# Kernel tuning notes

Hardware: AMD Instinct MI355X
Metric: run time of the kernel (lower is better)

The kernel has to match this reference:

```python
import math
import jax, jax.numpy as jnp
import numpy as np


def setup_inputs() -> dict:
    key = jax.random.key(0)
    k1, k2, k3, k4 = jax.random.split(key, 4)
    B, K, D = 131072, 64, 8
    NC = D * (D + 1) // 2  # 36
    pi = jax.random.uniform(k1, (B, K), dtype=jnp.float32)
    mu = jax.random.normal(k2, (K, D), dtype=jnp.float32)
    # 'ALREADY CONSTRAINED' Cholesky entries: keep them positive (uniform),
    # +0.1 offset keeps diagonal safely away from 0 for the log.
    L_constrained = jax.random.uniform(k3, (K, NC), dtype=jnp.float32) + 0.1
    target = jax.random.normal(k4, (B, D), dtype=jnp.float32)
    return {"pi": pi, "mu": mu, "L_constrained": L_constrained, "target": target}


def reference(pi, mu, L_constrained, target):
    B, K = pi.shape
    D = mu.shape[1]
    norm_const = -0.5 * D * math.log(2.0 * math.pi)
    ti, tj = np.tril_indices(D)
    # scatter packed cholesky into dense lower-triangular (K, D, D)
    L = jnp.zeros((K, D, D), dtype=target.dtype).at[:, ti, tj].set(L_constrained)
    diff = target[:, None, :] - mu[None, :, :]          # (B, K, D)
    # batch over components, treat B as multiple RHS: L (K,D,D) @ z = b (K,D,B)
    b = jnp.transpose(diff, (1, 2, 0))                   # (K, D, B)
    z = jax.scipy.linalg.solve_triangular(L, b, lower=True)  # (K, D, B)
    M = jnp.sum(z * z, axis=1)                           # (K, B) Mahalanobis^2
    log_dets = jnp.sum(jnp.log(jnp.diagonal(L, axis1=-2, axis2=-1)), axis=-1)  # (K,)
    log_probs = norm_const - log_dets[:, None] - 0.5 * M  # (K, B)
    weighted = log_probs.T + jnp.log(pi + 1e-10)          # (B, K)
    nll = -jnp.mean(jax.scipy.special.logsumexp(weighted, axis=1))
    return nll
```

## Files before the change

### kernel.cpp

```cpp
#include <hip/hip_runtime.h>
#include <math.h>

#define B_TOTAL 131072
#define K_COMP  64
#define D_DIM   8
#define NC      36
#define NFEAT   96
#define LPSI    104
#define ROWS_PB 128
#define TPW     2

#define NORM_CONST (-7.3515082656373815f)

typedef __attribute__((ext_vector_type(8))) short bf16x8;
typedef __attribute__((ext_vector_type(4))) float f32x4;

static __device__ __forceinline__ unsigned short bf16_rne(float x) {
    unsigned u = __float_as_uint(x);
    u += 0x7FFF + ((u >> 16) & 1);
    return (unsigned short)(u >> 16);
}
static __device__ __forceinline__ float bf16_f32(unsigned short h) {
    return __uint_as_float(((unsigned)h) << 16);
}

__global__ __launch_bounds__(256, 4) void mdn_fused(
        const float* __restrict__ pi,
        const float* __restrict__ mu,
        const float* __restrict__ Lc,
        const float* __restrict__ target,
        float* __restrict__ out) {
    const int tid = threadIdx.x;
    const int lane = tid & 63;
    const int w = tid >> 6;
    const int q = lane >> 4;
    const int n = lane & 15;
    const int rowbase = blockIdx.x * ROWS_PB;

    __shared__ __attribute__((aligned(16))) float Tl[ROWS_PB * D_DIM];
    __shared__ __attribute__((aligned(16))) unsigned short PsiH[K_COMP * LPSI];
    __shared__ __attribute__((aligned(16))) unsigned short PsiL[K_COMP * LPSI];

    ((float4*)Tl)[tid] = ((const float4*)(target + (size_t)rowbase * D_DIM))[tid];

    if (tid < K_COMP) {
        const int k = tid;
        const float* Lk = Lc + k * NC;

        float L[NC];
        float W[NC];
#pragma unroll
        for (int i = 0; i < NC; i++) L[i] = Lk[i];

        float logdet = 0.0f;
#pragma unroll
        for (int i = 0; i < D_DIM; i++) logdet += __logf(L[i * (i + 1) / 2 + i]);

#pragma unroll
        for (int j = 0; j < D_DIM; j++) {
            W[j * (j + 1) / 2 + j] = 1.0f / L[j * (j + 1) / 2 + j];
#pragma unroll
            for (int i = 0; i < D_DIM; i++) {
                if (i > j) {
                    float acc = 0.0f;
#pragma unroll
                    for (int m = 0; m < D_DIM; m++)
                        if (m >= j && m < i)
                            acc += L[i * (i + 1) / 2 + m] * W[m * (m + 1) / 2 + j];
                    W[i * (i + 1) / 2 + j] = -acc / L[i * (i + 1) / 2 + i];
                }
            }
        }

        float P[D_DIM][D_DIM];
#pragma unroll
        for (int a = 0; a < D_DIM; a++)
#pragma unroll
            for (int b = 0; b < D_DIM; b++) {
                float acc = 0.0f;
#pragma unroll
                for (int m = 0; m < D_DIM; m++)
                    if (m >= a && m >= b)
                        acc += W[m * (m + 1) / 2 + a] * W[m * (m + 1) / 2 + b];
                P[a][b] = acc;
            }

        float mv[D_DIM];
#pragma unroll
        for (int i = 0; i < D_DIM; i++) mv[i] = mu[k * D_DIM + i];

        float h[D_DIM];
        float qf = 0.0f;
#pragma unroll
        for (int i = 0; i < D_DIM; i++) {
            float acc = 0.0f;
#pragma unroll
            for (int j = 0; j < D_DIM; j++) acc += P[i][j] * mv[j];
            h[i] = acc;
            qf += mv[i] * acc;
        }
        float g = NORM_CONST - logdet - 0.5f * qf;

        float psi[NFEAT];
#pragma unroll
        for (int e = 0; e < NFEAT; e++) psi[e] = 0.0f;
#pragma unroll
        for (int a = 0; a < D_DIM; a++)
#pragma unroll
            for (int b = 0; b < D_DIM; b++) psi[8 * a + b] = -0.5f * P[a][b];
#pragma unroll
        for (int b = 0; b < D_DIM; b++) psi[64 + b] = h[b];
        psi[72] = g;

#pragma unroll
        for (int e8 = 0; e8 < NFEAT / 8; e8++) {
            bf16x8 vh, vl;
#pragma unroll
            for (int j = 0; j < 8; j++) {
                float v = psi[8 * e8 + j];
                unsigned short hi = bf16_rne(v);
                vh[j] = (short)hi;
                vl[j] = (short)bf16_rne(v - bf16_f32(hi));
            }
            *(bf16x8*)(PsiH + k * LPSI + 8 * e8) = vh;
            *(bf16x8*)(PsiL + k * LPSI + 8 * e8) = vl;
        }
    }
    __syncthreads();

    float lacc = 0.0f;

#pragma unroll 1
    for (int r = 0; r < TPW; r++) {
        const int row0 = (w * TPW + r) * 16;

        float pv[4][4];
#pragma unroll
        for (int reg = 0; reg < 4; reg++) {
            const float* pr = pi + (size_t)(rowbase + row0 + 4 * q + reg) * K_COMP + n;
#pragma unroll
            for (int nt = 0; nt < 4; nt++) pv[reg][nt] = pr[16 * nt];
        }

        const float4* trow = (const float4*)(Tl + (row0 + n) * D_DIM);
        float4 tlo = trow[0], thi = trow[1];
        float tv[D_DIM] = {tlo.x, tlo.y, tlo.z, tlo.w, thi.x, thi.y, thi.z, thi.w};

        float ta0 = (q & 2) ? ((q & 1) ? tlo.w : tlo.z) : ((q & 1) ? tlo.y : tlo.x);
        float ta1 = (q & 2) ? ((q & 1) ? thi.w : thi.z) : ((q & 1) ? thi.y : thi.x);

        bf16x8 Ahi[3], Alo[3];
#pragma unroll
        for (int j = 0; j < D_DIM; j++) {
            float f0 = ta0 * tv[j];
            unsigned short h0 = bf16_rne(f0);
            Ahi[0][j] = (short)h0;
            Alo[0][j] = (short)bf16_rne(f0 - bf16_f32(h0));

            float f1 = ta1 * tv[j];
            unsigned short h1 = bf16_rne(f1);
            Ahi[1][j] = (short)h1;
            Alo[1][j] = (short)bf16_rne(f1 - bf16_f32(h1));

            float f2 = (q == 0) ? tv[j] : ((q == 1 && j == 0) ? 1.0f : 0.0f);
            unsigned short h2 = bf16_rne(f2);
            Ahi[2][j] = (short)h2;
            Alo[2][j] = (short)bf16_rne(f2 - bf16_f32(h2));
        }

        f32x4 acc[4];
#pragma unroll
        for (int nt = 0; nt < 4; nt++) {
            const unsigned short* bh = PsiH + ((16 * nt + n) * LPSI + 8 * q);
            const unsigned short* bl = PsiL + ((16 * nt + n) * LPSI + 8 * q);
            f32x4 a = {0.0f, 0.0f, 0.0f, 0.0f};
#pragma unroll
            for (int ks = 0; ks < 3; ks++) {
                bf16x8 Bh = *(const bf16x8*)(bh + 32 * ks);
                bf16x8 Bl = *(const bf16x8*)(bl + 32 * ks);
                a = __builtin_amdgcn_mfma_f32_16x16x32_bf16(Ahi[ks], Bh, a, 0, 0, 0);
                a = __builtin_amdgcn_mfma_f32_16x16x32_bf16(Alo[ks], Bh, a, 0, 0, 0);
                a = __builtin_amdgcn_mfma_f32_16x16x32_bf16(Ahi[ks], Bl, a, 0, 0, 0);
            }
            acc[nt] = a;
        }

#pragma unroll
        for (int reg = 0; reg < 4; reg++) {
            float c0 = acc[0][reg], c1 = acc[1][reg], c2 = acc[2][reg], c3 = acc[3][reg];
            float mrow = fmaxf(fmaxf(c0, c1), fmaxf(c2, c3));
#pragma unroll
            for (int off = 1; off < 16; off <<= 1)
                mrow = fmaxf(mrow, __shfl_xor(mrow, off));
            float s = (pv[reg][0] + 1e-10f) * __expf(c0 - mrow)
                    + (pv[reg][1] + 1e-10f) * __expf(c1 - mrow)
                    + (pv[reg][2] + 1e-10f) * __expf(c2 - mrow)
                    + (pv[reg][3] + 1e-10f) * __expf(c3 - mrow);
#pragma unroll
            for (int off = 1; off < 16; off <<= 1)
                s += __shfl_xor(s, off);
            float lse = mrow + __logf(s);
            lacc += (n == 0) ? lse : 0.0f;
        }
    }

#pragma unroll
    for (int off = 32; off > 0; off >>= 1) lacc += __shfl_down(lacc, off);
    __shared__ float wsum[4];
    if (lane == 0) wsum[w] = lacc;
    __syncthreads();
    if (tid == 0) {
        atomicAdd(out, (wsum[0] + wsum[1] + wsum[2] + wsum[3]) * (-1.0f / (float)B_TOTAL));
    }
}

extern "C" void kernel_launch(void* const* d_in, const int* in_sizes, int n_in,
                              void* d_out, int out_size, void* d_ws, size_t ws_size,
                              hipStream_t stream) {
    const float* pi  = (const float*)d_in[0];
    const float* mu  = (const float*)d_in[1];
    const float* Lc  = (const float*)d_in[2];
    const float* tgt = (const float*)d_in[3];
    float* out = (float*)d_out;

    mdn_fused<<<B_TOTAL / ROWS_PB, 256, 0, stream>>>(pi, mu, Lc, tgt, out);
}
```

Before: 107.3 us.

## Split per-component precision-matrix precompute into a separate tiny kernel

```diff
diff --git a/kernel.cpp b/kernel.cpp
--- a/kernel.cpp
+++ b/kernel.cpp
@@ -7,6 +7,8 @@
 #define NC      36
 #define NFEAT   96
 #define LPSI    104
+#define PSI_SHORTS (K_COMP * LPSI)
+#define PSI_F4     (2 * PSI_SHORTS / 8)
 #define ROWS_PB 128
 #define TPW     2
 
@@ -24,10 +26,100 @@
     return __uint_as_float(((unsigned)h) << 16);
 }
 
-__global__ __launch_bounds__(256, 4) void mdn_fused(
+__global__ void mdn_precompute(const float* __restrict__ mu,
+                               const float* __restrict__ Lc,
+                               unsigned short* __restrict__ psig,
+                               float* __restrict__ out) {
+    const int k = threadIdx.x;
+    if (k == 0) out[0] = 0.0f;
+    if (k >= K_COMP) return;
+    const float* Lk = Lc + k * NC;
+
+    float L[NC];
+    float W[NC];
+#pragma unroll
+    for (int i = 0; i < NC; i++) L[i] = Lk[i];
+
+    float logdet = 0.0f;
+#pragma unroll
+    for (int i = 0; i < D_DIM; i++) logdet += __logf(L[i * (i + 1) / 2 + i]);
+
+#pragma unroll
+    for (int j = 0; j < D_DIM; j++) {
+        W[j * (j + 1) / 2 + j] = 1.0f / L[j * (j + 1) / 2 + j];
+#pragma unroll
+        for (int i = 0; i < D_DIM; i++) {
+            if (i > j) {
+                float acc = 0.0f;
+#pragma unroll
+                for (int m = 0; m < D_DIM; m++)
+                    if (m >= j && m < i)
+                        acc += L[i * (i + 1) / 2 + m] * W[m * (m + 1) / 2 + j];
+                W[i * (i + 1) / 2 + j] = -acc / L[i * (i + 1) / 2 + i];
+            }
+        }
+    }
+
+    float P[D_DIM][D_DIM];
+#pragma unroll
+    for (int a = 0; a < D_DIM; a++)
+#pragma unroll
+        for (int b = 0; b < D_DIM; b++) {
+            float acc = 0.0f;
+#pragma unroll
+            for (int m = 0; m < D_DIM; m++)
+                if (m >= a && m >= b)
+                    acc += W[m * (m + 1) / 2 + a] * W[m * (m + 1) / 2 + b];
+            P[a][b] = acc;
+        }
+
+    float mv[D_DIM];
+#pragma unroll
+    for (int i = 0; i < D_DIM; i++) mv[i] = mu[k * D_DIM + i];
+
+    float h[D_DIM];
+    float qf = 0.0f;
+#pragma unroll
+    for (int i = 0; i < D_DIM; i++) {
+        float acc = 0.0f;
+#pragma unroll
+        for (int j = 0; j < D_DIM; j++) acc += P[i][j] * mv[j];
+        h[i] = acc;
+        qf += mv[i] * acc;
+    }
+    float g = NORM_CONST - logdet - 0.5f * qf;
+
+    float psi[LPSI];
+#pragma unroll
+    for (int e = 0; e < LPSI; e++) psi[e] = 0.0f;
+#pragma unroll
+    for (int a = 0; a < D_DIM; a++)
+#pragma unroll
+        for (int b = 0; b < D_DIM; b++) psi[8 * a + b] = -0.5f * P[a][b];
+#pragma unroll
+    for (int b = 0; b < D_DIM; b++) psi[64 + b] = h[b];
+    psi[72] = g;
+
+    unsigned short* oh = psig + k * LPSI;
+    unsigned short* ol = psig + PSI_SHORTS + k * LPSI;
+#pragma unroll
+    for (int e8 = 0; e8 < LPSI / 8; e8++) {
+        bf16x8 vh, vl;
+#pragma unroll
+        for (int j = 0; j < 8; j++) {
+            float v = psi[8 * e8 + j];
+            unsigned short hi = bf16_rne(v);
+            vh[j] = (short)hi;
+            vl[j] = (short)bf16_rne(v - bf16_f32(hi));
+        }
+        *(bf16x8*)(oh + 8 * e8) = vh;
+        *(bf16x8*)(ol + 8 * e8) = vl;
+    }
+}
+
+__global__ __launch_bounds__(256, 4) void mdn_main(
         const float* __restrict__ pi,
-        const float* __restrict__ mu,
-        const float* __restrict__ Lc,
+        const unsigned short* __restrict__ psig,
         const float* __restrict__ target,
         float* __restrict__ out) {
     const int tid = threadIdx.x;
@@ -38,95 +130,23 @@
     const int rowbase = blockIdx.x * ROWS_PB;
 
     __shared__ __attribute__((aligned(16))) float Tl[ROWS_PB * D_DIM];
-    __shared__ __attribute__((aligned(16))) unsigned short PsiH[K_COMP * LPSI];
-    __shared__ __attribute__((aligned(16))) unsigned short PsiL[K_COMP * LPSI];
+    __shared__ __attribute__((aligned(16))) unsigned short Psi[2 * PSI_SHORTS];
 
     ((float4*)Tl)[tid] = ((const float4*)(target + (size_t)rowbase * D_DIM))[tid];
 
-    if (tid < K_COMP) {
-        const int k = tid;
-        const float* Lk = Lc + k * NC;
-
-        float L[NC];
-        float W[NC];
-#pragma unroll
-        for (int i = 0; i < NC; i++) L[i] = Lk[i];
-
-        float logdet = 0.0f;
-#pragma unroll
-        for (int i = 0; i < D_DIM; i++) logdet += __logf(L[i * (i + 1) / 2 + i]);
-
-#pragma unroll
-        for (int j = 0; j < D_DIM; j++) {
-            W[j * (j + 1) / 2 + j] = 1.0f / L[j * (j + 1) / 2 + j];
-#pragma unroll
-            for (int i = 0; i < D_DIM; i++) {
-                if (i > j) {
-                    float acc = 0.0f;
-#pragma unroll
-                    for (int m = 0; m < D_DIM; m++)
-                        if (m >= j && m < i)
-                            acc += L[i * (i + 1) / 2 + m] * W[m * (m + 1) / 2 + j];
-                    W[i * (i + 1) / 2 + j] = -acc / L[i * (i + 1) / 2 + i];
-                }
-            }
-        }
-
-        float P[D_DIM][D_DIM];
-#pragma unroll
-        for (int a = 0; a < D_DIM; a++)
-#pragma unroll
-            for (int b = 0; b < D_DIM; b++) {
-                float acc = 0.0f;
-#pragma unroll
-                for (int m = 0; m < D_DIM; m++)
-                    if (m >= a && m >= b)
-                        acc += W[m * (m + 1) / 2 + a] * W[m * (m + 1) / 2 + b];
-                P[a][b] = acc;
-            }
-
-        float mv[D_DIM];
-#pragma unroll
-        for (int i = 0; i < D_DIM; i++) mv[i] = mu[k * D_DIM + i];
-
-        float h[D_DIM];
-        float qf = 0.0f;
-#pragma unroll
-        for (int i = 0; i < D_DIM; i++) {
-            float acc = 0.0f;
-#pragma unroll
-            for (int j = 0; j < D_DIM; j++) acc += P[i][j] * mv[j];
-            h[i] = acc;
-            qf += mv[i] * acc;
-        }
-        float g = NORM_CONST - logdet - 0.5f * qf;
-
-        float psi[NFEAT];
-#pragma unroll
-        for (int e = 0; e < NFEAT; e++) psi[e] = 0.0f;
-#pragma unroll
-        for (int a = 0; a < D_DIM; a++)
-#pragma unroll
-            for (int b = 0; b < D_DIM; b++) psi[8 * a + b] = -0.5f * P[a][b];
-#pragma unroll
-        for (int b = 0; b < D_DIM; b++) psi[64 + b] = h[b];
-        psi[72] = g;
-
-#pragma unroll
-        for (int e8 = 0; e8 < NFEAT / 8; e8++) {
-            bf16x8 vh, vl;
-#pragma unroll
-            for (int j = 0; j < 8; j++) {
-                float v = psi[8 * e8 + j];
-                unsigned short hi = bf16_rne(v);
-                vh[j] = (short)hi;
-                vl[j] = (short)bf16_rne(v - bf16_f32(hi));
-            }
-            *(bf16x8*)(PsiH + k * LPSI + 8 * e8) = vh;
-            *(bf16x8*)(PsiL + k * LPSI + 8 * e8) = vl;
+    {
+        const float4* src = (const float4*)psig;
+        float4* dst = (float4*)Psi;
+#pragma unroll
+        for (int i = 0; i < 7; i++) {
+            const int idx = tid + 256 * i;
+            if (idx < PSI_F4) dst[idx] = src[idx];
         }
     }
     __syncthreads();
+
+    const unsigned short* PsiH = Psi;
+    const unsigned short* PsiL = Psi + PSI_SHORTS;
 
     float lacc = 0.0f;
 
@@ -222,6 +242,8 @@
     const float* Lc  = (const float*)d_in[2];
     const float* tgt = (const float*)d_in[3];
     float* out = (float*)d_out;
-
-    mdn_fused<<<B_TOTAL / ROWS_PB, 256, 0, stream>>>(pi, mu, Lc, tgt, out);
-}
+    unsigned short* psig = (unsigned short*)d_ws;
+
+    mdn_precompute<<<1, 64, 0, stream>>>(mu, Lc, psig, out);
+    mdn_main<<<B_TOTAL / ROWS_PB, 256, 0, stream>>>(pi, psig, tgt, out);
+}
```

Measured after the change: 111.4 us. 3.9% more time.
